# Kernel tuning notes

Hardware: AMD Instinct MI355X
Metric: run time of the kernel (lower is better)

The kernel has to match this reference:

```python
import jax, jax.numpy as jnp
import numpy as np
from jax import lax

EPS = 1e-12  # F.normalize default eps


def _l2_normalize(v, axis=-1):
    n = jnp.linalg.norm(v, axis=axis, keepdims=True)
    return v / jnp.maximum(n, EPS)


def setup_inputs() -> dict:
    key = jax.random.key(0)
    k1, k2, k3 = jax.random.split(key, 3)
    x = jax.random.normal(k1, (4, 768, 4096), dtype=jnp.float32)
    conv_w = jax.random.normal(k2, (128, 768, 3), dtype=jnp.float32) * 0.02
    codebook = jax.random.normal(k3, (8192, 128), dtype=jnp.float32)
    return {"x": x, "conv_w": conv_w, "codebook": codebook}


def reference(x, conv_w, codebook):
    # in_proj: Conv1d(input_dim -> codebook_dim, k=3, stride=2, pad=1, no bias)
    x_e = lax.conv_general_dilated(
        x, conv_w,
        window_strides=(2,), padding=[(1, 1)],
        dimension_numbers=("NCH", "OIH", "NCH"),
    )  # [b, d, t]
    b, d, t = x_e.shape
    enc = _l2_normalize(x_e.transpose(0, 2, 1).reshape(b * t, d))  # [(b t), d]
    cb = _l2_normalize(codebook)                                    # [K, d]
    # dist = ||e||^2 - 2 e.c + ||c||^2
    dist = (
        jnp.sum(enc * enc, axis=1, keepdims=True)
        - 2.0 * enc @ cb.T
        + jnp.sum(cb * cb, axis=1)[None, :]
    )  # [(b t), K]
    indices = jnp.argmax(-dist, axis=1).reshape(b, t)
    return indices
```

## Files before the change

kernel.cpp:

```cpp
#include <hip/hip_runtime.h>

#define EPS 1e-12f

#define BATCH 4
#define CIN   768
#define LIN   4096
#define DCODE 128
#define TOUT  2048
#define NROWS (BATCH*TOUT)
#define KCB   8192
#define KCONV 2304

#define OFF_CN2  0u
#define OFF_BS   32768u
#define OFF_BI   163840u
#define OFF_EH   294912u
#define OFF_EL   2392064u
#define OFF_CH   4489216u
#define OFF_CL   6586368u
#define OFF_WHT  8683520u
#define OFF_WLT  9273344u
#define OFF_PART 9863168u
#define OFF_XTH  18251776u
#define OFF_XTL  43417600u

typedef _Float16 half_t;
typedef __attribute__((ext_vector_type(8))) _Float16 half8;
typedef __attribute__((ext_vector_type(2))) _Float16 half2v;
typedef __attribute__((ext_vector_type(4))) float f32x4;

__global__ __launch_bounds__(256) void k_wt2(const float* __restrict__ w,
                                             half_t* __restrict__ wht,
                                             half_t* __restrict__ wlt) {
    int k = blockIdx.x * 256 + threadIdx.x;
    int n = blockIdx.y;
    if (k >= KCONV) return;
    int j = (k >= 1536) ? 2 : (k >= 768) ? 1 : 0;
    int c = k - j * 768;
    float v = w[(size_t)n * KCONV + c * 3 + j];
    half_t h = (half_t)v;
    wht[(size_t)n * KCONV + k] = h;
    wlt[(size_t)n * KCONV + k] = (half_t)(v - (float)h);
}

__global__ __launch_bounds__(256) void k_xt(const float* __restrict__ x,
                                            half_t* __restrict__ xth,
                                            half_t* __restrict__ xtl) {
    __shared__ float tile[32][33];
    const int s0 = blockIdx.x * 32;
    const int c0 = blockIdx.y * 32;
    const int b  = blockIdx.z;
    const int sl = threadIdx.x & 31;
    const int cl = threadIdx.x >> 5;
    const float* xg = x + ((size_t)b * CIN + c0) * LIN + s0;
    #pragma unroll
    for (int p = 0; p < 4; ++p) {
        int c = cl + p * 8;
        tile[c][sl] = xg[(size_t)c * LIN + sl];
    }
    __syncthreads();
    const int wcc = (threadIdx.x & 15) * 2;
    const int wss = threadIdx.x >> 4;
    #pragma unroll
    for (int p = 0; p < 2; ++p) {
        int s = wss + p * 16;
        float v0 = tile[wcc][s], v1 = tile[wcc + 1][s];
        half_t h0 = (half_t)v0, h1 = (half_t)v1;
        half_t l0 = (half_t)(v0 - (float)h0), l1 = (half_t)(v1 - (float)h1);
        size_t o = ((size_t)b * LIN + s0 + s) * CIN + c0 + wcc;
        *(half2v*)(xth + o) = half2v{h0, h1};
        *(half2v*)(xtl + o) = half2v{l0, l1};
    }
}

__global__ __launch_bounds__(256) void k_cbnorm(const float* __restrict__ cb,
                                                half_t* __restrict__ ch,
                                                half_t* __restrict__ cl,
                                                float* __restrict__ cn2) {
    int wid  = threadIdx.x >> 6;
    int lane = threadIdx.x & 63;
    int k = blockIdx.x * 4 + wid;
    const float2* src = (const float2*)cb + (size_t)k * 64;
    float2 v = src[lane];
    float ss = v.x * v.x + v.y * v.y;
    #pragma unroll
    for (int m = 1; m < 64; m <<= 1) ss += __shfl_xor(ss, m);
    float inv = 1.0f / fmaxf(sqrtf(ss), EPS);
    float nx = v.x * inv, ny = v.y * inv;
    half_t hx = (half_t)nx, hy = (half_t)ny;
    half_t lx = (half_t)(nx - (float)hx), ly = (half_t)(ny - (float)hy);
    ((half2v*)ch)[(size_t)k * 64 + lane] = half2v{hx, hy};
    ((half2v*)cl)[(size_t)k * 64 + lane] = half2v{lx, ly};
    if (lane == 0) cn2[k] = ss * inv * inv;
}

__global__ __launch_bounds__(512, 2) void k_conv_mfma(
        const half_t* __restrict__ xth, const half_t* __restrict__ xtl,
        const half_t* __restrict__ wht, const half_t* __restrict__ wlt,
        float* __restrict__ part) {
    extern __shared__ char smem[];
    const int tid  = threadIdx.x;
    const int lane = tid & 63;
    const int w    = tid >> 6;
    const int rg   = w >> 2;
    const int cgw  = w & 3;
    const int lr   = lane & 15;
    const int lg   = lane >> 4;
    const int r0   = blockIdx.x * 64;
    const int ks   = blockIdx.y;
    const int b    = r0 >> 11;
    const int t00  = r0 & 2047;
    const int kbase = ks * 1152;

    const half_t* msrc = (w >= 4) ? wlt : wht;
    const int wmod = w & 3;
    auto stage = [&](int t, int buf) {
        int k0 = kbase + t * 128;
        #pragma unroll
        for (int i = 0; i < 8; ++i) {
            int col_l = wmod * 32 + i * 4 + lg;
            int ksrc  = (lr * 16) ^ ((col_l & 7) << 4);
            const char* g = (const char*)msrc + (size_t)col_l * 4608
                          + (size_t)k0 * 2 + ksrc;
            char* l = smem + buf * 65536 + (w >> 2) * 32768 + wmod * 8192
                    + i * 1024;
            __builtin_amdgcn_global_load_lds(
                (const __attribute__((address_space(1))) void*)(uintptr_t)g,
                (__attribute__((address_space(3))) void*)(uintptr_t)l, 16, 0, 0);
        }
    };

    f32x4 acc[2][2];
    #pragma unroll
    for (int g = 0; g < 2; ++g)
        #pragma unroll
        for (int cg = 0; cg < 2; ++cg) acc[g][cg] = f32x4{0.f, 0.f, 0.f, 0.f};

    stage(0, 0);
    __syncthreads();

    int buf = 0;
    for (int t = 0; t < 9; ++t) {
        int k0 = kbase + t * 128;
        int j  = (k0 >= 1536) ? 2 : (k0 >= 768) ? 1 : 0;
        int c0 = k0 - j * 768;
        half8 ah[2][4], al[2][4];
        #pragma unroll
        for (int g = 0; g < 2; ++g) {
            int trow = t00 + rg * 32 + g * 16 + lr;
            int s = 2 * trow - 1 + j;
            bool valid = (unsigned)s < (unsigned)LIN;
            size_t o = ((size_t)b * LIN + (valid ? s : 0)) * CIN + c0 + lg * 8;
            const half8* ph = (const half8*)(xth + o);
            const half8* pl = (const half8*)(xtl + o);
            #pragma unroll
            for (int kc = 0; kc < 4; ++kc) {
                half8 vh = {}, vl = {};
                if (valid) { vh = ph[kc * 4]; vl = pl[kc * 4]; }
                ah[g][kc] = vh; al[g][kc] = vl;
            }
        }
        if (t < 8) stage(t + 1, buf ^ 1);
        const char* bhp = smem + buf * 65536;
        const char* blp = bhp + 32768;
        #pragma unroll
        for (int kc = 0; kc < 4; ++kc) {
            half8 bhf[2], blf[2];
            #pragma unroll
            for (int cg = 0; cg < 2; ++cg) {
                int col   = cgw * 32 + cg * 16 + lr;
                int kswz  = (col & 7) << 4;
                int cbyte = col * 256;
                int kb    = (kc * 64 + lg * 16) ^ kswz;
                bhf[cg] = *(const half8*)(bhp + cbyte + kb);
                blf[cg] = *(const half8*)(blp + cbyte + kb);
            }
            #pragma unroll
            for (int cg = 0; cg < 2; ++cg)
                #pragma unroll
                for (int g = 0; g < 2; ++g)
                    acc[g][cg] = __builtin_amdgcn_mfma_f32_16x16x32_f16(ah[g][kc], bhf[cg], acc[g][cg], 0, 0, 0);
            #pragma unroll
            for (int cg = 0; cg < 2; ++cg)
                #pragma unroll
                for (int g = 0; g < 2; ++g)
                    acc[g][cg] = __builtin_amdgcn_mfma_f32_16x16x32_f16(al[g][kc], bhf[cg], acc[g][cg], 0, 0, 0);
            #pragma unroll
            for (int cg = 0; cg < 2; ++cg)
                #pragma unroll
                for (int g = 0; g < 2; ++g)
                    acc[g][cg] = __builtin_amdgcn_mfma_f32_16x16x32_f16(ah[g][kc], blf[cg], acc[g][cg], 0, 0, 0);
        }
        __syncthreads();
        buf ^= 1;
    }

    float* pb = part + (size_t)ks * NROWS * DCODE;
    #pragma unroll
    for (int g = 0; g < 2; ++g)
        #pragma unroll
        for (int cg = 0; cg < 2; ++cg) {
            int col = cgw * 32 + cg * 16 + lr;
            #pragma unroll
            for (int rr = 0; rr < 4; ++rr) {
                int row = r0 + rg * 32 + g * 16 + lg * 4 + rr;
                pb[(size_t)row * DCODE + col] = acc[g][cg][rr];
            }
        }
}

__global__ __launch_bounds__(256) void k_encnorm(const float* __restrict__ part,
                                                 half_t* __restrict__ eh,
                                                 half_t* __restrict__ el) {
    int wid  = threadIdx.x >> 6;
    int lane = threadIdx.x & 63;
    int r = blockIdx.x * 4 + wid;
    const float2* p0 = (const float2*)part + (size_t)r * 64;
    const float2* p1 = (const float2*)(part + (size_t)NROWS * DCODE) + (size_t)r * 64;
    float2 a = p0[lane];
    float2 c = p1[lane];
    a.x += c.x; a.y += c.y;
    float ss = a.x * a.x + a.y * a.y;
    #pragma unroll
    for (int m = 1; m < 64; m <<= 1) ss += __shfl_xor(ss, m);
    float inv = 1.0f / fmaxf(sqrtf(ss), EPS);
    float nx = a.x * inv, ny = a.y * inv;
    half_t hx = (half_t)nx, hy = (half_t)ny;
    half_t lx = (half_t)(nx - (float)hx), ly = (half_t)(ny - (float)hy);
    ((half2v*)eh)[(size_t)r * 64 + lane] = half2v{hx, hy};
    ((half2v*)el)[(size_t)r * 64 + lane] = half2v{lx, ly};
}

__global__ __launch_bounds__(512, 2) void k_dist(const half_t* __restrict__ eh,
                                                 const half_t* __restrict__ el,
                                                 const half_t* __restrict__ ch,
                                                 const half_t* __restrict__ cl,
                                                 const float* __restrict__ cn2,
                                                 float* __restrict__ best_s,
                                                 int* __restrict__ best_i) {
    extern __shared__ char smem[];
    const int tid  = threadIdx.x;
    const int lane = tid & 63;
    const int w    = tid >> 6;
    const int lr   = lane & 15;
    const int lg   = lane >> 4;
    const int r0   = blockIdx.x * 64;
    const int kqbase = blockIdx.y * 4096;

    half8 ah[4][4], al[4][4];
    #pragma unroll
    for (int g = 0; g < 4; ++g) {
        int row = r0 + g * 16 + lr;
        const half8* ph = (const half8*)(eh + (size_t)row * 128 + lg * 8);
        const half8* pl = (const half8*)(el + (size_t)row * 128 + lg * 8);
        #pragma unroll
        for (int kc = 0; kc < 4; ++kc) { ah[g][kc] = ph[kc * 4]; al[g][kc] = pl[kc * 4]; }
    }

    const half_t* msrc = (w >= 4) ? cl : ch;
    const int wmod = w & 3;
    auto stage = [&](int t, int buf) {
        #pragma unroll
        for (int i = 0; i < 8; ++i) {
            int col_l = wmod * 32 + i * 4 + lg;
            int ksrc  = (lr * 16) ^ ((col_l & 7) << 4);
            const char* g = (const char*)msrc
                          + ((size_t)(kqbase + t * 128 + col_l)) * 256 + ksrc;
            char* l = smem + buf * 65536 + (w >> 2) * 32768 + wmod * 8192
                    + i * 1024;
            __builtin_amdgcn_global_load_lds(
                (const __attribute__((address_space(1))) void*)(uintptr_t)g,
                (__attribute__((address_space(3))) void*)(uintptr_t)l, 16, 0, 0);
        }
    };

    float bs[4][4]; int bi[4][4];
    #pragma unroll
    for (int g = 0; g < 4; ++g)
        #pragma unroll
        for (int rr = 0; rr < 4; ++rr) { bs[g][rr] = -3.4e38f; bi[g][rr] = 0; }

    stage(0, 0);
    __syncthreads();

    int buf = 0;
    for (int t = 0; t < 32; ++t) {
        if (t < 31) stage(t + 1, buf ^ 1);
        int n = kqbase + t * 128 + w * 16 + lr;
        float cnv = cn2[n];
        const char* bhp = smem + buf * 65536;
        const char* blp = bhp + 32768;
        f32x4 acc[4];
        #pragma unroll
        for (int g = 0; g < 4; ++g) acc[g] = f32x4{0.f, 0.f, 0.f, 0.f};
        const int col   = w * 16 + lr;
        const int kswz  = (col & 7) << 4;
        const int cbyte = col * 256;
        #pragma unroll
        for (int kc = 0; kc < 4; ++kc) {
            int kb = (kc * 64 + lg * 16) ^ kswz;
            half8 bhf = *(const half8*)(bhp + cbyte + kb);
            half8 blf = *(const half8*)(blp + cbyte + kb);
            #pragma unroll
            for (int g = 0; g < 4; ++g)
                acc[g] = __builtin_amdgcn_mfma_f32_16x16x32_f16(ah[g][kc], bhf, acc[g], 0, 0, 0);
            #pragma unroll
            for (int g = 0; g < 4; ++g)
                acc[g] = __builtin_amdgcn_mfma_f32_16x16x32_f16(al[g][kc], bhf, acc[g], 0, 0, 0);
            #pragma unroll
            for (int g = 0; g < 4; ++g)
                acc[g] = __builtin_amdgcn_mfma_f32_16x16x32_f16(ah[g][kc], blf, acc[g], 0, 0, 0);
        }
        #pragma unroll
        for (int g = 0; g < 4; ++g)
            #pragma unroll
            for (int rr = 0; rr < 4; ++rr) {
                float sc = 2.0f * acc[g][rr] - cnv;
                if (sc > bs[g][rr]) { bs[g][rr] = sc; bi[g][rr] = n; }
            }
        __syncthreads();
        buf ^= 1;
    }

    float* redS = (float*)smem;
    int*   redI = (int*)(smem + 2048);
    #pragma unroll
    for (int g = 0; g < 4; ++g)
        #pragma unroll
        for (int rr = 0; rr < 4; ++rr) {
            float s = bs[g][rr]; int i = bi[g][rr];
            #pragma unroll
            for (int m = 1; m < 16; m <<= 1) {
                float os = __shfl_xor(s, m);
                int   oi = __shfl_xor(i, m);
                if (os > s || (os == s && oi < i)) { s = os; i = oi; }
            }
            if (lr == 0) {
                int row = g * 16 + lg * 4 + rr;
                redS[w * 64 + row] = s;
                redI[w * 64 + row] = i;
            }
        }
    __syncthreads();
    if (tid < 64) {
        float s = redS[tid]; int i = redI[tid];
        #pragma unroll
        for (int w2 = 1; w2 < 8; ++w2) {
            float s2 = redS[w2 * 64 + tid];
            int   i2 = redI[w2 * 64 + tid];
            if (s2 > s || (s2 == s && i2 < i)) { s = s2; i = i2; }
        }
        best_s[(size_t)blockIdx.y * NROWS + r0 + tid] = s;
        best_i[(size_t)blockIdx.y * NROWS + r0 + tid] = i;
    }
}

__global__ __launch_bounds__(256) void k_merge(const float* __restrict__ bs,
                                               const int* __restrict__ bi,
                                               int* __restrict__ out) {
    int r = blockIdx.x * 256 + threadIdx.x;
    if (r >= NROWS) return;
    float s = bs[r]; int i = bi[r];
    #pragma unroll
    for (int q = 1; q < 2; ++q) {
        float s2 = bs[(size_t)q * NROWS + r];
        int   i2 = bi[(size_t)q * NROWS + r];
        if (s2 > s || (s2 == s && i2 < i)) { s = s2; i = i2; }
    }
    out[r] = i;
}

extern "C" void kernel_launch(void* const* d_in, const int* in_sizes, int n_in,
                              void* d_out, int out_size, void* d_ws, size_t ws_size,
                              hipStream_t stream) {
    const float* x  = (const float*)d_in[0];
    const float* w  = (const float*)d_in[1];
    const float* cb = (const float*)d_in[2];
    char* ws = (char*)d_ws;
    float*  cn2  = (float*)(ws + OFF_CN2);
    float*  bs   = (float*)(ws + OFF_BS);
    int*    bi   = (int*)(ws + OFF_BI);
    half_t* eh   = (half_t*)(ws + OFF_EH);
    half_t* el   = (half_t*)(ws + OFF_EL);
    half_t* chh  = (half_t*)(ws + OFF_CH);
    half_t* cll  = (half_t*)(ws + OFF_CL);
    half_t* wht  = (half_t*)(ws + OFF_WHT);
    half_t* wlt  = (half_t*)(ws + OFF_WLT);
    float*  part = (float*)(ws + OFF_PART);
    half_t* xth  = (half_t*)(ws + OFF_XTH);
    half_t* xtl  = (half_t*)(ws + OFF_XTL);
    int*    out  = (int*)d_out;

    hipFuncSetAttribute((const void*)k_dist,
                        hipFuncAttributeMaxDynamicSharedMemorySize, 131072);
    hipFuncSetAttribute((const void*)k_conv_mfma,
                        hipFuncAttributeMaxDynamicSharedMemorySize, 131072);

    k_wt2     <<<dim3(9, 128), 256, 0, stream>>>(w, wht, wlt);
    k_cbnorm  <<<2048, 256, 0, stream>>>(cb, chh, cll, cn2);
    k_xt      <<<dim3(128, 24, 4), 256, 0, stream>>>(x, xth, xtl);
    k_conv_mfma<<<dim3(128, 2), 512, 131072, stream>>>(xth, xtl, wht, wlt, part);
    k_encnorm <<<2048, 256, 0, stream>>>(part, eh, el);
    k_dist    <<<dim3(128, 2), 512, 131072, stream>>>(eh, el, chh, cll, cn2, bs, bi);
    k_merge   <<<32, 256, 0, stream>>>(bs, bi, out);
}
```

Before: 212.4 us.

## Widen x transpose tiles and deepen k_dist codebook pipeline with 2x2 warp tiling

The x transpose kernel now uses 64x128 tiles with float4 loads and half8 stores, cutting the number of blocks and widening memory transactions. The distance kernel reorganizes warps into a 2x2 row/column tile so each warp holds half the A fragments and reuses B fragments across two row groups. It also replaces the per-iteration __syncthreads with explicit vmcnt waits and raw barriers so two stages of codebook loads can be in flight, and caches codebook norms in LDS. LDS use rises to 144KB per block, which may limit occupancy to one block per CU. The hand-placed waitcnt and barrier scheme is also fragile.

```diff
diff --git a/kernel.cpp b/kernel.cpp
--- a/kernel.cpp
+++ b/kernel.cpp
@@ -29,6 +29,8 @@
 typedef __attribute__((ext_vector_type(2))) _Float16 half2v;
 typedef __attribute__((ext_vector_type(4))) float f32x4;
 
+#define VMCNT(n) asm volatile("s_waitcnt vmcnt(" #n ")" ::: "memory")
+
 __global__ __launch_bounds__(256) void k_wt2(const float* __restrict__ w,
                                              half_t* __restrict__ wht,
                                              half_t* __restrict__ wlt) {
@@ -46,30 +48,36 @@
 __global__ __launch_bounds__(256) void k_xt(const float* __restrict__ x,
                                             half_t* __restrict__ xth,
                                             half_t* __restrict__ xtl) {
-    __shared__ float tile[32][33];
-    const int s0 = blockIdx.x * 32;
-    const int c0 = blockIdx.y * 32;
+    __shared__ float tile[128 * 68];
+    const int s0 = blockIdx.x * 64;
+    const int c0 = blockIdx.y * 128;
     const int b  = blockIdx.z;
-    const int sl = threadIdx.x & 31;
-    const int cl = threadIdx.x >> 5;
-    const float* xg = x + ((size_t)b * CIN + c0) * LIN + s0;
-    #pragma unroll
-    for (int p = 0; p < 4; ++p) {
-        int c = cl + p * 8;
-        tile[c][sl] = xg[(size_t)c * LIN + sl];
+    const int f4  = threadIdx.x & 15;
+    const int crb = threadIdx.x >> 4;
+    #pragma unroll
+    for (int p = 0; p < 8; ++p) {
+        int cr = crb + p * 16;
+        float4 v = *(const float4*)(x + ((size_t)(b * CIN + c0 + cr)) * LIN + s0 + f4 * 4);
+        *(float4*)(tile + cr * 68 + f4 * 4) = v;
     }
     __syncthreads();
-    const int wcc = (threadIdx.x & 15) * 2;
-    const int wss = threadIdx.x >> 4;
-    #pragma unroll
-    for (int p = 0; p < 2; ++p) {
-        int s = wss + p * 16;
-        float v0 = tile[wcc][s], v1 = tile[wcc + 1][s];
-        half_t h0 = (half_t)v0, h1 = (half_t)v1;
-        half_t l0 = (half_t)(v0 - (float)h0), l1 = (half_t)(v1 - (float)h1);
-        size_t o = ((size_t)b * LIN + s0 + s) * CIN + c0 + wcc;
-        *(half2v*)(xth + o) = half2v{h0, h1};
-        *(half2v*)(xtl + o) = half2v{l0, l1};
+    const int sr = threadIdx.x >> 2;
+    const int cq = threadIdx.x & 3;
+    size_t ob = ((size_t)b * LIN + s0 + sr) * CIN + c0 + cq * 32;
+    half8 hv[4], lv[4];
+    #pragma unroll
+    for (int q = 0; q < 4; ++q)
+        #pragma unroll
+        for (int e = 0; e < 8; ++e) {
+            float v = tile[(cq * 32 + q * 8 + e) * 68 + sr];
+            half_t h = (half_t)v;
+            hv[q][e] = h;
+            lv[q][e] = (half_t)(v - (float)h);
+        }
+    #pragma unroll
+    for (int q = 0; q < 4; ++q) {
+        *(half8*)(xth + ob + q * 8) = hv[q];
+        *(half8*)(xtl + ob + q * 8) = lv[q];
     }
 }
 
@@ -242,15 +250,21 @@
     const int tid  = threadIdx.x;
     const int lane = tid & 63;
     const int w    = tid >> 6;
+    const int rg   = w >> 2;
+    const int cgw  = w & 3;
     const int lr   = lane & 15;
     const int lg   = lane >> 4;
     const int r0   = blockIdx.x * 64;
     const int kqbase = blockIdx.y * 4096;
 
-    half8 ah[4][4], al[4][4];
-    #pragma unroll
-    for (int g = 0; g < 4; ++g) {
-        int row = r0 + g * 16 + lr;
+    float* cnS = (float*)(smem + 131072);
+    for (int i = tid; i < 1024; i += 512)
+        ((float4*)cnS)[i] = ((const float4*)(cn2 + kqbase))[i];
+
+    half8 ah[2][4], al[2][4];
+    #pragma unroll
+    for (int g = 0; g < 2; ++g) {
+        int row = r0 + rg * 32 + g * 16 + lr;
         const half8* ph = (const half8*)(eh + (size_t)row * 128 + lg * 8);
         const half8* pl = (const half8*)(el + (size_t)row * 128 + lg * 8);
         #pragma unroll
@@ -274,58 +288,78 @@
         }
     };
 
-    float bs[4][4]; int bi[4][4];
-    #pragma unroll
-    for (int g = 0; g < 4; ++g)
+    float bs[2][4]; int bi[2][4];
+    #pragma unroll
+    for (int g = 0; g < 2; ++g)
         #pragma unroll
         for (int rr = 0; rr < 4; ++rr) { bs[g][rr] = -3.4e38f; bi[g][rr] = 0; }
 
     stage(0, 0);
+    stage(1, 1);
     __syncthreads();
 
     int buf = 0;
+    const int colb = cgw * 32;
     for (int t = 0; t < 32; ++t) {
-        if (t < 31) stage(t + 1, buf ^ 1);
-        int n = kqbase + t * 128 + w * 16 + lr;
-        float cnv = cn2[n];
+        if (t >= 2) {
+            if (t < 31) { VMCNT(8); } else { VMCNT(0); }
+            __builtin_amdgcn_s_barrier();
+            __builtin_amdgcn_sched_barrier(0);
+        }
         const char* bhp = smem + buf * 65536;
         const char* blp = bhp + 32768;
-        f32x4 acc[4];
-        #pragma unroll
-        for (int g = 0; g < 4; ++g) acc[g] = f32x4{0.f, 0.f, 0.f, 0.f};
-        const int col   = w * 16 + lr;
-        const int kswz  = (col & 7) << 4;
-        const int cbyte = col * 256;
+        f32x4 acc[2][2];
+        #pragma unroll
+        for (int g = 0; g < 2; ++g)
+            #pragma unroll
+            for (int cg = 0; cg < 2; ++cg) acc[g][cg] = f32x4{0.f, 0.f, 0.f, 0.f};
         #pragma unroll
         for (int kc = 0; kc < 4; ++kc) {
-            int kb = (kc * 64 + lg * 16) ^ kswz;
-            half8 bhf = *(const half8*)(bhp + cbyte + kb);
-            half8 blf = *(const half8*)(blp + cbyte + kb);
-            #pragma unroll
-            for (int g = 0; g < 4; ++g)
-                acc[g] = __builtin_amdgcn_mfma_f32_16x16x32_f16(ah[g][kc], bhf, acc[g], 0, 0, 0);
-            #pragma unroll
-            for (int g = 0; g < 4; ++g)
-                acc[g] = __builtin_amdgcn_mfma_f32_16x16x32_f16(al[g][kc], bhf, acc[g], 0, 0, 0);
-            #pragma unroll
-            for (int g = 0; g < 4; ++g)
-                acc[g] = __builtin_amdgcn_mfma_f32_16x16x32_f16(ah[g][kc], blf, acc[g], 0, 0, 0);
-        }
-        #pragma unroll
-        for (int g = 0; g < 4; ++g)
-            #pragma unroll
-            for (int rr = 0; rr < 4; ++rr) {
-                float sc = 2.0f * acc[g][rr] - cnv;
-                if (sc > bs[g][rr]) { bs[g][rr] = sc; bi[g][rr] = n; }
-            }
-        __syncthreads();
+            half8 bhf[2], blf[2];
+            #pragma unroll
+            for (int cg = 0; cg < 2; ++cg) {
+                int col = colb + cg * 16 + lr;
+                int kb  = (kc * 64 + lg * 16) ^ ((col & 7) << 4);
+                bhf[cg] = *(const half8*)(bhp + col * 256 + kb);
+                blf[cg] = *(const half8*)(blp + col * 256 + kb);
+            }
+            #pragma unroll
+            for (int cg = 0; cg < 2; ++cg)
+                #pragma unroll
+                for (int g = 0; g < 2; ++g)
+                    acc[g][cg] = __builtin_amdgcn_mfma_f32_16x16x32_f16(ah[g][kc], bhf[cg], acc[g][cg], 0, 0, 0);
+            #pragma unroll
+            for (int cg = 0; cg < 2; ++cg)
+                #pragma unroll
+                for (int g = 0; g < 2; ++g)
+                    acc[g][cg] = __builtin_amdgcn_mfma_f32_16x16x32_f16(al[g][kc], bhf[cg], acc[g][cg], 0, 0, 0);
+            #pragma unroll
+            for (int cg = 0; cg < 2; ++cg)
+                #pragma unroll
+                for (int g = 0; g < 2; ++g)
+                    acc[g][cg] = __builtin_amdgcn_mfma_f32_16x16x32_f16(ah[g][kc], blf[cg], acc[g][cg], 0, 0, 0);
+        }
+        #pragma unroll
+        for (int g = 0; g < 2; ++g)
+            #pragma unroll
+            for (int cg = 0; cg < 2; ++cg) {
+                float cnv = cnS[t * 128 + colb + cg * 16 + lr];
+                int n = kqbase + t * 128 + colb + cg * 16 + lr;
+                #pragma unroll
+                for (int rr = 0; rr < 4; ++rr) {
+                    float sc = 2.0f * acc[g][cg][rr] - cnv;
+                    if (sc > bs[g][rr]) { bs[g][rr] = sc; bi[g][rr] = n; }
+                }
+            }
+        __builtin_amdgcn_s_barrier();
+        if (t + 2 < 32) stage(t + 2, buf);
         buf ^= 1;
     }
 
     float* redS = (float*)smem;
-    int*   redI = (int*)(smem + 2048);
-    #pragma unroll
-    for (int g = 0; g < 4; ++g)
+    int*   redI = (int*)(smem + 1024);
+    #pragma unroll
+    for (int g = 0; g < 2; ++g)
         #pragma unroll
         for (int rr = 0; rr < 4; ++rr) {
             float s = bs[g][rr]; int i = bi[g][rr];
@@ -336,18 +370,20 @@
                 if (os > s || (os == s && oi < i)) { s = os; i = oi; }
             }
             if (lr == 0) {
-                int row = g * 16 + lg * 4 + rr;
-                redS[w * 64 + row] = s;
-                redI[w * 64 + row] = i;
+                int rloc = g * 16 + lg * 4 + rr;
+                redS[w * 32 + rloc] = s;
+                redI[w * 32 + rloc] = i;
             }
         }
     __syncthreads();
     if (tid < 64) {
-        float s = redS[tid]; int i = redI[tid];
-        #pragma unroll
-        for (int w2 = 1; w2 < 8; ++w2) {
-            float s2 = redS[w2 * 64 + tid];
-            int   i2 = redI[w2 * 64 + tid];
+        int rgg = tid >> 5, rloc = tid & 31;
+        float s = redS[(rgg * 4) * 32 + rloc];
+        int   i = redI[(rgg * 4) * 32 + rloc];
+        #pragma unroll
+        for (int j = 1; j < 4; ++j) {
+            float s2 = redS[(rgg * 4 + j) * 32 + rloc];
+            int   i2 = redI[(rgg * 4 + j) * 32 + rloc];
             if (s2 > s || (s2 == s && i2 < i)) { s = s2; i = i2; }
         }
         best_s[(size_t)blockIdx.y * NROWS + r0 + tid] = s;
@@ -392,15 +428,15 @@
     int*    out  = (int*)d_out;
 
     hipFuncSetAttribute((const void*)k_dist,
-                        hipFuncAttributeMaxDynamicSharedMemorySize, 131072);
+                        hipFuncAttributeMaxDynamicSharedMemorySize, 147456);
     hipFuncSetAttribute((const void*)k_conv_mfma,
                         hipFuncAttributeMaxDynamicSharedMemorySize, 131072);
 
     k_wt2     <<<dim3(9, 128), 256, 0, stream>>>(w, wht, wlt);
     k_cbnorm  <<<2048, 256, 0, stream>>>(cb, chh, cll, cn2);
-    k_xt      <<<dim3(128, 24, 4), 256, 0, stream>>>(x, xth, xtl);
+    k_xt      <<<dim3(64, 6, 4), 256, 0, stream>>>(x, xth, xtl);
     k_conv_mfma<<<dim3(128, 2), 512, 131072, stream>>>(xth, xtl, wht, wlt, part);
     k_encnorm <<<2048, 256, 0, stream>>>(part, eh, el);
-    k_dist    <<<dim3(128, 2), 512, 131072, stream>>>(eh, el, chh, cll, cn2, bs, bi);
+    k_dist    <<<dim3(128, 2), 512, 147456, stream>>>(eh, el, chh, cll, cn2, bs, bi);
     k_merge   <<<32, 256, 0, stream>>>(bs, bi, out);
 }
```

New measurement: 212.3 us. No clear change (-0.0%).

## Deepen k_dist prefetch pipeline and widen transpose tiles in k_xt

Applied to the files above, without the earlier changes.

k_dist now stages two codebook tiles ahead, using explicit vmcnt waits and raw s_barrier in place of a full __syncthreads after each issue. The codebook norms are cached in shared memory, and the encoder fragments are loaded with inline-asm global loads. k_xt switches to 128x64 tiles with float4 reads and half8 writes, which cuts block count and widens memory transactions. The extra LDS brings k_dist to 144 KiB, which may limit occupancy. Hand-written vmcnt counts are fragile if the compiler reorders or adds memory ops.

```diff
diff --git a/kernel.cpp b/kernel.cpp
--- a/kernel.cpp
+++ b/kernel.cpp
@@ -29,6 +29,10 @@
 typedef __attribute__((ext_vector_type(2))) _Float16 half2v;
 typedef __attribute__((ext_vector_type(4))) float f32x4;
 
+#define VMCNT(n) asm volatile("s_waitcnt vmcnt(" #n ")" ::: "memory")
+#define ALOAD(dst, p) asm volatile("global_load_dwordx4 %0, %1, off" \
+                                   : "=&v"(dst) : "v"(p))
+
 __global__ __launch_bounds__(256) void k_wt2(const float* __restrict__ w,
                                              half_t* __restrict__ wht,
                                              half_t* __restrict__ wlt) {
@@ -46,30 +50,36 @@
 __global__ __launch_bounds__(256) void k_xt(const float* __restrict__ x,
                                             half_t* __restrict__ xth,
                                             half_t* __restrict__ xtl) {
-    __shared__ float tile[32][33];
-    const int s0 = blockIdx.x * 32;
-    const int c0 = blockIdx.y * 32;
+    __shared__ float tile[128 * 68];
+    const int s0 = blockIdx.x * 64;
+    const int c0 = blockIdx.y * 128;
     const int b  = blockIdx.z;
-    const int sl = threadIdx.x & 31;
-    const int cl = threadIdx.x >> 5;
-    const float* xg = x + ((size_t)b * CIN + c0) * LIN + s0;
-    #pragma unroll
-    for (int p = 0; p < 4; ++p) {
-        int c = cl + p * 8;
-        tile[c][sl] = xg[(size_t)c * LIN + sl];
+    const int f4  = threadIdx.x & 15;
+    const int crb = threadIdx.x >> 4;
+    #pragma unroll
+    for (int p = 0; p < 8; ++p) {
+        int cr = crb + p * 16;
+        float4 v = *(const float4*)(x + ((size_t)(b * CIN + c0 + cr)) * LIN + s0 + f4 * 4);
+        *(float4*)(tile + cr * 68 + f4 * 4) = v;
     }
     __syncthreads();
-    const int wcc = (threadIdx.x & 15) * 2;
-    const int wss = threadIdx.x >> 4;
-    #pragma unroll
-    for (int p = 0; p < 2; ++p) {
-        int s = wss + p * 16;
-        float v0 = tile[wcc][s], v1 = tile[wcc + 1][s];
-        half_t h0 = (half_t)v0, h1 = (half_t)v1;
-        half_t l0 = (half_t)(v0 - (float)h0), l1 = (half_t)(v1 - (float)h1);
-        size_t o = ((size_t)b * LIN + s0 + s) * CIN + c0 + wcc;
-        *(half2v*)(xth + o) = half2v{h0, h1};
-        *(half2v*)(xtl + o) = half2v{l0, l1};
+    const int sr = threadIdx.x >> 2;
+    const int cq = threadIdx.x & 3;
+    size_t ob = ((size_t)b * LIN + s0 + sr) * CIN + c0 + cq * 32;
+    half8 hv[4], lv[4];
+    #pragma unroll
+    for (int q = 0; q < 4; ++q)
+        #pragma unroll
+        for (int e = 0; e < 8; ++e) {
+            float v = tile[(cq * 32 + q * 8 + e) * 68 + sr];
+            half_t h = (half_t)v;
+            hv[q][e] = h;
+            lv[q][e] = (half_t)(v - (float)h);
+        }
+    #pragma unroll
+    for (int q = 0; q < 4; ++q) {
+        *(half8*)(xth + ob + q * 8) = hv[q];
+        *(half8*)(xtl + ob + q * 8) = lv[q];
     }
 }
 
@@ -247,14 +257,21 @@
     const int r0   = blockIdx.x * 64;
     const int kqbase = blockIdx.y * 4096;
 
+    float* cnS = (float*)(smem + 131072);
+    for (int i = tid; i < 1024; i += 512)
+        ((float4*)cnS)[i] = ((const float4*)(cn2 + kqbase))[i];
+
     half8 ah[4][4], al[4][4];
     #pragma unroll
     for (int g = 0; g < 4; ++g) {
         int row = r0 + g * 16 + lr;
-        const half8* ph = (const half8*)(eh + (size_t)row * 128 + lg * 8);
-        const half8* pl = (const half8*)(el + (size_t)row * 128 + lg * 8);
-        #pragma unroll
-        for (int kc = 0; kc < 4; ++kc) { ah[g][kc] = ph[kc * 4]; al[g][kc] = pl[kc * 4]; }
+        const half_t* ph = eh + (size_t)row * 128 + lg * 8;
+        const half_t* pl = el + (size_t)row * 128 + lg * 8;
+        #pragma unroll
+        for (int kc = 0; kc < 4; ++kc) {
+            ALOAD(ah[g][kc], ph + kc * 32);
+            ALOAD(al[g][kc], pl + kc * 32);
+        }
     }
 
     const half_t* msrc = (w >= 4) ? cl : ch;
@@ -281,21 +298,26 @@
         for (int rr = 0; rr < 4; ++rr) { bs[g][rr] = -3.4e38f; bi[g][rr] = 0; }
 
     stage(0, 0);
+    stage(1, 1);
+    VMCNT(0);
     __syncthreads();
 
     int buf = 0;
+    const int colb = w * 16;
+    const int col  = colb + lr;
+    const int kswz = (col & 7) << 4;
+    const int cbyte = col * 256;
     for (int t = 0; t < 32; ++t) {
-        if (t < 31) stage(t + 1, buf ^ 1);
-        int n = kqbase + t * 128 + w * 16 + lr;
-        float cnv = cn2[n];
+        if (t >= 2) {
+            if (t < 31) { VMCNT(8); } else { VMCNT(0); }
+            __builtin_amdgcn_s_barrier();
+            __builtin_amdgcn_sched_barrier(0);
+        }
         const char* bhp = smem + buf * 65536;
         const char* blp = bhp + 32768;
         f32x4 acc[4];
         #pragma unroll
         for (int g = 0; g < 4; ++g) acc[g] = f32x4{0.f, 0.f, 0.f, 0.f};
-        const int col   = w * 16 + lr;
-        const int kswz  = (col & 7) << 4;
-        const int cbyte = col * 256;
         #pragma unroll
         for (int kc = 0; kc < 4; ++kc) {
             int kb = (kc * 64 + lg * 16) ^ kswz;
@@ -311,14 +333,19 @@
             for (int g = 0; g < 4; ++g)
                 acc[g] = __builtin_amdgcn_mfma_f32_16x16x32_f16(ah[g][kc], blf, acc[g], 0, 0, 0);
         }
-        #pragma unroll
-        for (int g = 0; g < 4; ++g)
-            #pragma unroll
-            for (int rr = 0; rr < 4; ++rr) {
-                float sc = 2.0f * acc[g][rr] - cnv;
-                if (sc > bs[g][rr]) { bs[g][rr] = sc; bi[g][rr] = n; }
-            }
-        __syncthreads();
+        {
+            int n = kqbase + t * 128 + col;
+            float cnv = cnS[t * 128 + col];
+            #pragma unroll
+            for (int g = 0; g < 4; ++g)
+                #pragma unroll
+                for (int rr = 0; rr < 4; ++rr) {
+                    float sc = 2.0f * acc[g][rr] - cnv;
+                    if (sc > bs[g][rr]) { bs[g][rr] = sc; bi[g][rr] = n; }
+                }
+        }
+        __builtin_amdgcn_s_barrier();
+        if (t + 2 < 32) stage(t + 2, buf);
         buf ^= 1;
     }
 
@@ -392,15 +419,15 @@
     int*    out  = (int*)d_out;
 
     hipFuncSetAttribute((const void*)k_dist,
-                        hipFuncAttributeMaxDynamicSharedMemorySize, 131072);
+                        hipFuncAttributeMaxDynamicSharedMemorySize, 147456);
     hipFuncSetAttribute((const void*)k_conv_mfma,
                         hipFuncAttributeMaxDynamicSharedMemorySize, 131072);
 
     k_wt2     <<<dim3(9, 128), 256, 0, stream>>>(w, wht, wlt);
     k_cbnorm  <<<2048, 256, 0, stream>>>(cb, chh, cll, cn2);
-    k_xt      <<<dim3(128, 24, 4), 256, 0, stream>>>(x, xth, xtl);
+    k_xt      <<<dim3(64, 6, 4), 256, 0, stream>>>(x, xth, xtl);
     k_conv_mfma<<<dim3(128, 2), 512, 131072, stream>>>(xth, xtl, wht, wlt, part);
     k_encnorm <<<2048, 256, 0, stream>>>(part, eh, el);
-    k_dist    <<<dim3(128, 2), 512, 131072, stream>>>(eh, el, chh, cll, cn2, bs, bi);
+    k_dist    <<<dim3(128, 2), 512, 147456, stream>>>(eh, el, chh, cll, cn2, bs, bi);
     k_merge   <<<32, 256, 0, stream>>>(bs, bi, out);
 }
```

After: 217.9 us. 1.03x slower.
